# Kernel optimization log

Hardware: AMD Instinct MI355X
Metric: run time of the kernel (lower is better)

## Reference

```python
import jax, jax.numpy as jnp
import numpy as np

E = 1024
H = 8
D = E // H
B = 16384
LN_EPS = 1e-5


def setup_inputs() -> dict:
    key = jax.random.key(0)
    ks = jax.random.split(key, 12)
    s = 1.0 / np.sqrt(E)
    return {
        "image_features": jax.random.normal(ks[0], (B, E), jnp.float32),
        "signal_features": jax.random.normal(ks[1], (B, E), jnp.float32),
        "Wq": jax.random.normal(ks[2], (E, E), jnp.float32) * s,
        "Wk": jax.random.normal(ks[3], (E, E), jnp.float32) * s,
        "Wv": jax.random.normal(ks[4], (E, E), jnp.float32) * s,
        "bq": jnp.zeros((E,), jnp.float32),
        "bk": jnp.zeros((E,), jnp.float32),
        "bv": jnp.zeros((E,), jnp.float32),
        "Wo": jax.random.normal(ks[5], (E, E), jnp.float32) * s,
        "bo": jnp.zeros((E,), jnp.float32),
        "ln_gamma": jnp.ones((E,), jnp.float32),
        "ln_beta": jnp.zeros((E,), jnp.float32),
    }


def _forward(image_features, signal_features, Wq, Wk, Wv, bq, bk, bv, Wo, bo, ln_gamma, ln_beta):
    # query: [B,1,E] from image; key/value: [B,2,E] stacked modalities
    kv = jnp.stack([image_features, signal_features], axis=1)  # [B,2,E]
    # projections (torch Linear convention: x @ W^T + b)
    q = (image_features @ Wq.T + bq).reshape(B, H, 1, D)       # [B,H,1,D]
    k = (kv @ Wk.T + bk).reshape(B, 2, H, D).transpose(0, 2, 1, 3)  # [B,H,2,D]
    v = (kv @ Wv.T + bv).reshape(B, 2, H, D).transpose(0, 2, 1, 3)  # [B,H,2,D]
    scale = 1.0 / jnp.sqrt(jnp.float32(D))
    scores = jnp.einsum("bhqd,bhkd->bhqk", q, k) * scale       # [B,H,1,2]
    attn = jax.nn.softmax(scores, axis=-1)
    ctx = jnp.einsum("bhqk,bhkd->bhqd", attn, v)               # [B,H,1,D]
    ctx = ctx.reshape(B, E)
    attn_out = ctx @ Wo.T + bo
    # residual + LayerNorm (dropout is identity in eval)
    fused = attn_out + image_features
    mu = jnp.mean(fused, axis=-1, keepdims=True)
    var = jnp.var(fused, axis=-1, keepdims=True)
    normed = (fused - mu) * jax.lax.rsqrt(var + LN_EPS)
    return normed * ln_gamma + ln_beta


def reference(image_features, signal_features, Wq, Wk, Wv, bq, bk, bv, Wo, bo, ln_gamma, ln_beta):
    return _forward(image_features, signal_features, Wq, Wk, Wv, bq, bk, bv, Wo, bo, ln_gamma, ln_beta)
```

## Files before the change

### kernel.cpp

```cpp
#include <hip/hip_runtime.h>

#define B_ 16384
#define E_ 1024
#define H_ 8
#define D_ 128

typedef _Float16 f16;
typedef _Float16 f16x8 __attribute__((ext_vector_type(8)));
typedef float f32x4 __attribute__((ext_vector_type(4)));

__device__ __forceinline__ void gload16(const f16* g, f16* l) {
    __builtin_amdgcn_global_load_lds(
        (const __attribute__((address_space(1))) void*)g,
        (__attribute__((address_space(3))) void*)l, 16, 0, 0);
}


__global__ __launch_bounds__(256) void cvt2_kernel(const float4* __restrict__ s0,
                                                   const float4* __restrict__ s1,
                                                   ushort4* __restrict__ d0,
                                                   ushort4* __restrict__ d1, int n4) {
    const float4* s = blockIdx.y ? s1 : s0;
    ushort4* d = blockIdx.y ? d1 : d0;
    int i = blockIdx.x * 256 + threadIdx.x;
    if (i >= n4) return;
    float4 v = s[i];
    union { ushort4 u; f16 h[4]; } o;
    o.h[0] = (f16)v.x; o.h[1] = (f16)v.y; o.h[2] = (f16)v.z; o.h[3] = (f16)v.w;
    d[i] = o.u;
}

__global__ __launch_bounds__(256) void cvt4_kernel(
    const float4* __restrict__ s0, const float4* __restrict__ s1,
    const float4* __restrict__ s2, const float4* __restrict__ s3,
    ushort4* __restrict__ d0, ushort4* __restrict__ d1,
    ushort4* __restrict__ d2, ushort4* __restrict__ d3, int n4) {
    const float4* s; ushort4* d;
    switch (blockIdx.y) {
        case 0: s = s0; d = d0; break;
        case 1: s = s1; d = d1; break;
        case 2: s = s2; d = d2; break;
        default: s = s3; d = d3; break;
    }
    int i = blockIdx.x * 256 + threadIdx.x;
    if (i >= n4) return;
    float4 v = s[i];
    union { ushort4 u; f16 h[4]; } o;
    o.h[0] = (f16)v.x; o.h[1] = (f16)v.y; o.h[2] = (f16)v.z; o.h[3] = (f16)v.w;
    d[i] = o.u;
}

__global__ __launch_bounds__(256, 2) void qkv_attn_kernel(
    const f16* __restrict__ Xi, const f16* __restrict__ Xs,
    const f16* __restrict__ Wq, const f16* __restrict__ Wk, const f16* __restrict__ Wv,
    const float* __restrict__ bq, const float* __restrict__ bk, const float* __restrict__ bv,
    f16* __restrict__ ctx)
{
    (void)bk;
    __shared__ f16 sAi[2][64][32];
    __shared__ f16 sAs[2][64][32];
    __shared__ f16 sWq[2][128][32];
    __shared__ f16 sWk[2][128][32];
    __shared__ f16 sWv[2][128][32];
    __shared__ float sdot[64][2];
    __shared__ float sa0[64];

    const int tid  = threadIdx.x;
    const int lane = tid & 63;
    const int wave = tid >> 6;
    const int wr = wave >> 1, wc = wave & 1;
    const int l16 = lane & 15, lq = lane >> 4;

    const int bid  = blockIdx.x;
    const int head = bid & 7;
    const int row0 = (bid >> 3) * 64;
    const int col0 = head * D_;

    const int lr = lane >> 2;
    const int lc = ((lane & 3) ^ ((lane >> 3) & 3)) * 8;
    const int rc = (lq ^ ((l16 >> 1) & 3)) * 8;

    const f16* gAi = Xi + (size_t)(row0 + wave * 16 + lr) * E_ + lc;
    const f16* gAs = Xs + (size_t)(row0 + wave * 16 + lr) * E_ + lc;
    const size_t woff = (size_t)(col0 + wave * 32 + lr) * E_ + lc;
    const f16* gWq = Wq + woff;
    const f16* gWk = Wk + woff;
    const f16* gWv = Wv + woff;
    const size_t wskip = (size_t)16 * E_;

    f32x4 zero4 = {0.f, 0.f, 0.f, 0.f};
    f32x4 accQ[2][4], accKd[2][4], accVd[2][4], accVs[2][4];
    #pragma unroll
    for (int i = 0; i < 2; i++)
        #pragma unroll
        for (int j = 0; j < 4; j++) {
            accQ[i][j] = zero4; accKd[i][j] = zero4;
            accVd[i][j] = zero4; accVs[i][j] = zero4;
        }

    for (int kk = 0; kk < E_; kk += 64) {
        #pragma unroll
        for (int h = 0; h < 2; h++) {
            const int ko = kk + h * 32;
            gload16(gAi + ko,         &sAi[h][wave * 16][0]);
            gload16(gAs + ko,         &sAs[h][wave * 16][0]);
            gload16(gWq + ko,         &sWq[h][wave * 32][0]);
            gload16(gWq + wskip + ko, &sWq[h][wave * 32 + 16][0]);
            gload16(gWk + ko,         &sWk[h][wave * 32][0]);
            gload16(gWk + wskip + ko, &sWk[h][wave * 32 + 16][0]);
            gload16(gWv + ko,         &sWv[h][wave * 32][0]);
            gload16(gWv + wskip + ko, &sWv[h][wave * 32 + 16][0]);
        }
        __syncthreads();

        #pragma unroll
        for (int h = 0; h < 2; h++) {
            f16x8 aI[2], aS[2], aD[2], bF[4];
            #pragma unroll
            for (int fr = 0; fr < 2; fr++) {
                aI[fr] = *(const f16x8*)&sAi[h][wr * 32 + fr * 16 + l16][rc];
                aS[fr] = *(const f16x8*)&sAs[h][wr * 32 + fr * 16 + l16][rc];
                aD[fr] = aI[fr] - aS[fr];
            }
            #pragma unroll
            for (int fc = 0; fc < 4; fc++)
                bF[fc] = *(const f16x8*)&sWq[h][wc * 64 + fc * 16 + l16][rc];
            #pragma unroll
            for (int fr = 0; fr < 2; fr++)
                #pragma unroll
                for (int fc = 0; fc < 4; fc++)
                    accQ[fr][fc] = __builtin_amdgcn_mfma_f32_16x16x32_f16(aI[fr], bF[fc], accQ[fr][fc], 0, 0, 0);
            #pragma unroll
            for (int fc = 0; fc < 4; fc++)
                bF[fc] = *(const f16x8*)&sWk[h][wc * 64 + fc * 16 + l16][rc];
            #pragma unroll
            for (int fr = 0; fr < 2; fr++)
                #pragma unroll
                for (int fc = 0; fc < 4; fc++)
                    accKd[fr][fc] = __builtin_amdgcn_mfma_f32_16x16x32_f16(aD[fr], bF[fc], accKd[fr][fc], 0, 0, 0);
            #pragma unroll
            for (int fc = 0; fc < 4; fc++)
                bF[fc] = *(const f16x8*)&sWv[h][wc * 64 + fc * 16 + l16][rc];
            #pragma unroll
            for (int fr = 0; fr < 2; fr++)
                #pragma unroll
                for (int fc = 0; fc < 4; fc++) {
                    accVs[fr][fc] = __builtin_amdgcn_mfma_f32_16x16x32_f16(aS[fr], bF[fc], accVs[fr][fc], 0, 0, 0);
                    accVd[fr][fc] = __builtin_amdgcn_mfma_f32_16x16x32_f16(aD[fr], bF[fc], accVd[fr][fc], 0, 0, 0);
                }
        }
        __syncthreads();
    }

    #pragma unroll
    for (int fc = 0; fc < 4; fc++) {
        int col = col0 + wc * 64 + fc * 16 + l16;
        float bqv = bq[col];
        #pragma unroll
        for (int fr = 0; fr < 2; fr++)
            #pragma unroll
            for (int e = 0; e < 4; e++)
                accQ[fr][fc][e] += bqv;
    }

    #pragma unroll
    for (int fr = 0; fr < 2; fr++)
        #pragma unroll
        for (int e = 0; e < 4; e++) {
            float d = 0.f;
            #pragma unroll
            for (int fc = 0; fc < 4; fc++)
                d += accQ[fr][fc][e] * accKd[fr][fc][e];
            #pragma unroll
            for (int m = 1; m < 16; m <<= 1)
                d += __shfl_xor(d, m, 64);
            if (l16 == 0) {
                int row = wr * 32 + fr * 16 + lq * 4 + e;
                sdot[row][wc] = d;
            }
        }
    __syncthreads();
    if (tid < 64) {
        const float scale = 0.088388347648318447f;
        float delta = (sdot[tid][0] + sdot[tid][1]) * scale;
        sa0[tid] = 1.0f / (1.0f + expf(-delta));
    }
    __syncthreads();

    #pragma unroll
    for (int fc = 0; fc < 4; fc++) {
        int col = col0 + wc * 64 + fc * 16 + l16;
        float bvv = bv[col];
        #pragma unroll
        for (int fr = 0; fr < 2; fr++)
            #pragma unroll
            for (int e = 0; e < 4; e++) {
                int row = wr * 32 + fr * 16 + lq * 4 + e;
                float a0 = sa0[row];
                float v  = fmaf(a0, accVd[fr][fc][e], accVs[fr][fc][e]) + bvv;
                ctx[(size_t)(row0 + row) * E_ + col] = (f16)v;
            }
    }
}

__global__ __launch_bounds__(256, 4) void out_proj_kernel(
    const f16* __restrict__ A, const f16* __restrict__ Wo, const float* __restrict__ bo,
    f16* __restrict__ a16)
{
    __shared__ f16 sA[2][128][32];
    __shared__ f16 sB[2][128][32];
    const int tid  = threadIdx.x;
    const int lane = tid & 63;
    const int wave = tid >> 6;
    const int wr = wave >> 1, wc = wave & 1;
    const int l16 = lane & 15, lq = lane >> 4;

    const int bid  = blockIdx.x;
    const int col0 = (bid & 7) * 128;
    const int row0 = (bid >> 3) * 128;

    const int lr = lane >> 2;
    const int lc = ((lane & 3) ^ ((lane >> 3) & 3)) * 8;
    const int rc = (lq ^ ((l16 >> 1) & 3)) * 8;

    const f16* gA0 = A  + (size_t)(row0 + wave * 32 + lr) * E_ + lc;
    const f16* gB0 = Wo + (size_t)(col0 + wave * 32 + lr) * E_ + lc;
    const size_t wskip = (size_t)16 * E_;

    f32x4 zero4 = {0.f, 0.f, 0.f, 0.f};
    f32x4 acc[4][4];
    #pragma unroll
    for (int i = 0; i < 4; i++)
        #pragma unroll
        for (int j = 0; j < 4; j++) acc[i][j] = zero4;

    for (int kk = 0; kk < E_; kk += 64) {
        #pragma unroll
        for (int h = 0; h < 2; h++) {
            const int ko = kk + h * 32;
            gload16(gA0 + ko,         &sA[h][wave * 32][0]);
            gload16(gA0 + wskip + ko, &sA[h][wave * 32 + 16][0]);
            gload16(gB0 + ko,         &sB[h][wave * 32][0]);
            gload16(gB0 + wskip + ko, &sB[h][wave * 32 + 16][0]);
        }
        __syncthreads();

        #pragma unroll
        for (int h = 0; h < 2; h++) {
            f16x8 aF[4], bF[4];
            #pragma unroll
            for (int f = 0; f < 4; f++) {
                aF[f] = *(const f16x8*)&sA[h][wr * 64 + f * 16 + l16][rc];
                bF[f] = *(const f16x8*)&sB[h][wc * 64 + f * 16 + l16][rc];
            }
            #pragma unroll
            for (int fr = 0; fr < 4; fr++)
                #pragma unroll
                for (int fc = 0; fc < 4; fc++)
                    acc[fr][fc] = __builtin_amdgcn_mfma_f32_16x16x32_f16(aF[fr], bF[fc], acc[fr][fc], 0, 0, 0);
        }
        __syncthreads();
    }

    #pragma unroll
    for (int fc = 0; fc < 4; fc++) {
        int col = col0 + wc * 64 + fc * 16 + l16;
        float bov = bo[col];
        #pragma unroll
        for (int fr = 0; fr < 4; fr++)
            #pragma unroll
            for (int e = 0; e < 4; e++) {
                int row = row0 + wr * 64 + fr * 16 + lq * 4 + e;
                a16[(size_t)row * E_ + col] = (f16)(acc[fr][fc][e] + bov);
            }
    }
}

__global__ __launch_bounds__(256) void ln_kernel(
    const f16* __restrict__ a16, const f16* __restrict__ resid16,
    const float* __restrict__ gamma, const float* __restrict__ beta,
    float* __restrict__ out)
{
    const int row = blockIdx.x;
    const int tid = threadIdx.x;
    union { ushort4 u; f16 h[4]; } ua, ur;
    ua.u = ((const ushort4*)(a16     + (size_t)row * E_))[tid];
    ur.u = ((const ushort4*)(resid16 + (size_t)row * E_))[tid];
    float4 v;
    v.x = (float)ua.h[0] + (float)ur.h[0];
    v.y = (float)ua.h[1] + (float)ur.h[1];
    v.z = (float)ua.h[2] + (float)ur.h[2];
    v.w = (float)ua.h[3] + (float)ur.h[3];
    float s  = v.x + v.y + v.z + v.w;
    float s2 = v.x * v.x + v.y * v.y + v.z * v.z + v.w * v.w;
    #pragma unroll
    for (int m = 1; m < 64; m <<= 1) {
        s  += __shfl_xor(s, m, 64);
        s2 += __shfl_xor(s2, m, 64);
    }
    __shared__ float red[8];
    int wv = tid >> 6, ln = tid & 63;
    if (ln == 0) { red[wv] = s; red[4 + wv] = s2; }
    __syncthreads();
    s  = red[0] + red[1] + red[2] + red[3];
    s2 = red[4] + red[5] + red[6] + red[7];
    float mu  = s * (1.0f / E_);
    float var = s2 * (1.0f / E_) - mu * mu;
    float r   = rsqrtf(var + 1e-5f);
    float4 g  = ((const float4*)gamma)[tid];
    float4 bb = ((const float4*)beta)[tid];
    float4 o;
    o.x = (v.x - mu) * r * g.x + bb.x;
    o.y = (v.y - mu) * r * g.y + bb.y;
    o.z = (v.z - mu) * r * g.z + bb.z;
    o.w = (v.w - mu) * r * g.w + bb.w;
    ((float4*)(out + (size_t)row * E_))[tid] = o;
}

extern "C" void kernel_launch(void* const* d_in, const int* in_sizes, int n_in,
                              void* d_out, int out_size, void* d_ws, size_t ws_size,
                              hipStream_t stream)
{
    (void)in_sizes; (void)n_in; (void)out_size; (void)ws_size;
    const float* image  = (const float*)d_in[0];
    const float* signal = (const float*)d_in[1];
    const float* Wq = (const float*)d_in[2];
    const float* Wk = (const float*)d_in[3];
    const float* Wv = (const float*)d_in[4];
    const float* bq = (const float*)d_in[5];
    const float* bk = (const float*)d_in[6];
    const float* bv = (const float*)d_in[7];
    const float* Wo = (const float*)d_in[8];
    const float* bo = (const float*)d_in[9];
    const float* gamma = (const float*)d_in[10];
    const float* beta  = (const float*)d_in[11];
    float* out = (float*)d_out;

    char* ws = (char*)d_ws;
    f16* Xi16 = (f16*)(ws);
    f16* Xs16 = (f16*)(ws + 32ull * 1024 * 1024);
    f16* Wq16 = (f16*)(ws + 64ull * 1024 * 1024);
    f16* Wk16 = (f16*)(ws + 66ull * 1024 * 1024);
    f16* Wv16 = (f16*)(ws + 68ull * 1024 * 1024);
    f16* Wo16 = (f16*)(ws + 70ull * 1024 * 1024);
    f16* ctx  = (f16*)(ws + 72ull * 1024 * 1024);
    f16* a16  = Xs16;

    const int nBE4 = B_ * E_ / 4;
    const int nEE4 = E_ * E_ / 4;
    dim3 gX(nBE4 / 256, 2);
    cvt2_kernel<<<gX, 256, 0, stream>>>((const float4*)image, (const float4*)signal,
                                        (ushort4*)Xi16, (ushort4*)Xs16, nBE4);
    dim3 gW(nEE4 / 256, 4);
    cvt4_kernel<<<gW, 256, 0, stream>>>((const float4*)Wq, (const float4*)Wk,
                                        (const float4*)Wv, (const float4*)Wo,
                                        (ushort4*)Wq16, (ushort4*)Wk16,
                                        (ushort4*)Wv16, (ushort4*)Wo16, nEE4);

    qkv_attn_kernel<<<B_ / 64 * H_, 256, 0, stream>>>(Xi16, Xs16, Wq16, Wk16, Wv16,
                                                      bq, bk, bv, ctx);

    out_proj_kernel<<<B_ / 128 * 8, 256, 0, stream>>>(ctx, Wo16, bo, a16);

    ln_kernel<<<B_, 256, 0, stream>>>(a16, Xi16, gamma, beta, out);
}
```

Before: 430.4 us.

## Fuse fp32-to-fp16 activation conversion into QKV GEMM tile loads

Removes the separate conversion kernel for image and signal features. The QKV kernel now reads fp32 activations directly, converts them in registers and writes swizzled fp16 tiles to LDS. LayerNorm reads the fp32 residual. The grid changes to 2D, putting heads on blockIdx.y, which changes block scheduling order and how the activation tiles are shared across the 8 head blocks in L2. This removes the 64MB read plus 32MB write conversion pass. The cost is that each of the 8 head blocks rereads fp32 activations at twice the bytes and loses the async global_load_lds path for those tiles.

Measured after the change: 446.6 us. +3.8%, slower.

```diff
diff --git a/kernel.cpp b/kernel.cpp
--- a/kernel.cpp
+++ b/kernel.cpp
@@ -15,20 +15,6 @@
         (__attribute__((address_space(3))) void*)l, 16, 0, 0);
 }
 
-
-__global__ __launch_bounds__(256) void cvt2_kernel(const float4* __restrict__ s0,
-                                                   const float4* __restrict__ s1,
-                                                   ushort4* __restrict__ d0,
-                                                   ushort4* __restrict__ d1, int n4) {
-    const float4* s = blockIdx.y ? s1 : s0;
-    ushort4* d = blockIdx.y ? d1 : d0;
-    int i = blockIdx.x * 256 + threadIdx.x;
-    if (i >= n4) return;
-    float4 v = s[i];
-    union { ushort4 u; f16 h[4]; } o;
-    o.h[0] = (f16)v.x; o.h[1] = (f16)v.y; o.h[2] = (f16)v.z; o.h[3] = (f16)v.w;
-    d[i] = o.u;
-}
 
 __global__ __launch_bounds__(256) void cvt4_kernel(
     const float4* __restrict__ s0, const float4* __restrict__ s1,
@@ -51,7 +37,7 @@
 }
 
 __global__ __launch_bounds__(256, 2) void qkv_attn_kernel(
-    const f16* __restrict__ Xi, const f16* __restrict__ Xs,
+    const float* __restrict__ Xi, const float* __restrict__ Xs,
     const f16* __restrict__ Wq, const f16* __restrict__ Wk, const f16* __restrict__ Wv,
     const float* __restrict__ bq, const float* __restrict__ bk, const float* __restrict__ bv,
     f16* __restrict__ ctx)
@@ -71,17 +57,18 @@
     const int wr = wave >> 1, wc = wave & 1;
     const int l16 = lane & 15, lq = lane >> 4;
 
-    const int bid  = blockIdx.x;
-    const int head = bid & 7;
-    const int row0 = (bid >> 3) * 64;
-    const int col0 = head * D_;
+    const int row0 = blockIdx.x * 64;
+    const int col0 = blockIdx.y * D_;
 
     const int lr = lane >> 2;
     const int lc = ((lane & 3) ^ ((lane >> 3) & 3)) * 8;
     const int rc = (lq ^ ((l16 >> 1) & 3)) * 8;
 
-    const f16* gAi = Xi + (size_t)(row0 + wave * 16 + lr) * E_ + lc;
-    const f16* gAs = Xs + (size_t)(row0 + wave * 16 + lr) * E_ + lc;
+    const int xchunk = ((lane & 3) ^ ((lr >> 1) & 3)) * 8;
+    const float* gAif = Xi + (size_t)(row0 + wave * 16 + lr) * E_ + xchunk;
+    const float* gAsf = Xs + (size_t)(row0 + wave * 16 + lr) * E_ + xchunk;
+    const int ldst = (lane & 3) * 8;
+
     const size_t woff = (size_t)(col0 + wave * 32 + lr) * E_ + lc;
     const f16* gWq = Wq + woff;
     const f16* gWk = Wk + woff;
@@ -102,14 +89,27 @@
         #pragma unroll
         for (int h = 0; h < 2; h++) {
             const int ko = kk + h * 32;
-            gload16(gAi + ko,         &sAi[h][wave * 16][0]);
-            gload16(gAs + ko,         &sAs[h][wave * 16][0]);
             gload16(gWq + ko,         &sWq[h][wave * 32][0]);
             gload16(gWq + wskip + ko, &sWq[h][wave * 32 + 16][0]);
             gload16(gWk + ko,         &sWk[h][wave * 32][0]);
             gload16(gWk + wskip + ko, &sWk[h][wave * 32 + 16][0]);
             gload16(gWv + ko,         &sWv[h][wave * 32][0]);
             gload16(gWv + wskip + ko, &sWv[h][wave * 32 + 16][0]);
+        }
+        #pragma unroll
+        for (int h = 0; h < 2; h++) {
+            const int ko = kk + h * 32;
+            float4 i0 = *(const float4*)&gAif[ko];
+            float4 i1 = *(const float4*)&gAif[ko + 4];
+            float4 s0 = *(const float4*)&gAsf[ko];
+            float4 s1 = *(const float4*)&gAsf[ko + 4];
+            union { uint4 u; f16 hh[8]; } ui, us;
+            ui.hh[0] = (f16)i0.x; ui.hh[1] = (f16)i0.y; ui.hh[2] = (f16)i0.z; ui.hh[3] = (f16)i0.w;
+            ui.hh[4] = (f16)i1.x; ui.hh[5] = (f16)i1.y; ui.hh[6] = (f16)i1.z; ui.hh[7] = (f16)i1.w;
+            us.hh[0] = (f16)s0.x; us.hh[1] = (f16)s0.y; us.hh[2] = (f16)s0.z; us.hh[3] = (f16)s0.w;
+            us.hh[4] = (f16)s1.x; us.hh[5] = (f16)s1.y; us.hh[6] = (f16)s1.z; us.hh[7] = (f16)s1.w;
+            *(uint4*)&sAi[h][wave * 16 + lr][ldst] = ui.u;
+            *(uint4*)&sAs[h][wave * 16 + lr][ldst] = us.u;
         }
         __syncthreads();
 
@@ -277,20 +277,20 @@
 }
 
 __global__ __launch_bounds__(256) void ln_kernel(
-    const f16* __restrict__ a16, const f16* __restrict__ resid16,
+    const f16* __restrict__ a16, const float* __restrict__ resid,
     const float* __restrict__ gamma, const float* __restrict__ beta,
     float* __restrict__ out)
 {
     const int row = blockIdx.x;
     const int tid = threadIdx.x;
-    union { ushort4 u; f16 h[4]; } ua, ur;
-    ua.u = ((const ushort4*)(a16     + (size_t)row * E_))[tid];
-    ur.u = ((const ushort4*)(resid16 + (size_t)row * E_))[tid];
+    union { ushort4 u; f16 h[4]; } ua;
+    ua.u = ((const ushort4*)(a16 + (size_t)row * E_))[tid];
+    float4 rv = ((const float4*)(resid + (size_t)row * E_))[tid];
     float4 v;
-    v.x = (float)ua.h[0] + (float)ur.h[0];
-    v.y = (float)ua.h[1] + (float)ur.h[1];
-    v.z = (float)ua.h[2] + (float)ur.h[2];
-    v.w = (float)ua.h[3] + (float)ur.h[3];
+    v.x = (float)ua.h[0] + rv.x;
+    v.y = (float)ua.h[1] + rv.y;
+    v.z = (float)ua.h[2] + rv.z;
+    v.w = (float)ua.h[3] + rv.w;
     float s  = v.x + v.y + v.z + v.w;
     float s2 = v.x * v.x + v.y * v.y + v.z * v.z + v.w * v.w;
     #pragma unroll
@@ -337,30 +337,25 @@
     float* out = (float*)d_out;
 
     char* ws = (char*)d_ws;
-    f16* Xi16 = (f16*)(ws);
-    f16* Xs16 = (f16*)(ws + 32ull * 1024 * 1024);
-    f16* Wq16 = (f16*)(ws + 64ull * 1024 * 1024);
-    f16* Wk16 = (f16*)(ws + 66ull * 1024 * 1024);
-    f16* Wv16 = (f16*)(ws + 68ull * 1024 * 1024);
-    f16* Wo16 = (f16*)(ws + 70ull * 1024 * 1024);
-    f16* ctx  = (f16*)(ws + 72ull * 1024 * 1024);
-    f16* a16  = Xs16;
-
-    const int nBE4 = B_ * E_ / 4;
+    f16* Wq16 = (f16*)(ws);
+    f16* Wk16 = (f16*)(ws + 2ull  * 1024 * 1024);
+    f16* Wv16 = (f16*)(ws + 4ull  * 1024 * 1024);
+    f16* Wo16 = (f16*)(ws + 6ull  * 1024 * 1024);
+    f16* ctx  = (f16*)(ws + 8ull  * 1024 * 1024);
+    f16* a16  = (f16*)(ws + 40ull * 1024 * 1024);
+
     const int nEE4 = E_ * E_ / 4;
-    dim3 gX(nBE4 / 256, 2);
-    cvt2_kernel<<<gX, 256, 0, stream>>>((const float4*)image, (const float4*)signal,
-                                        (ushort4*)Xi16, (ushort4*)Xs16, nBE4);
     dim3 gW(nEE4 / 256, 4);
     cvt4_kernel<<<gW, 256, 0, stream>>>((const float4*)Wq, (const float4*)Wk,
                                         (const float4*)Wv, (const float4*)Wo,
                                         (ushort4*)Wq16, (ushort4*)Wk16,
                                         (ushort4*)Wv16, (ushort4*)Wo16, nEE4);
 
-    qkv_attn_kernel<<<B_ / 64 * H_, 256, 0, stream>>>(Xi16, Xs16, Wq16, Wk16, Wv16,
-                                                      bq, bk, bv, ctx);
+    dim3 g2(B_ / 64, H_);
+    qkv_attn_kernel<<<g2, 256, 0, stream>>>(image, signal, Wq16, Wk16, Wv16,
+                                            bq, bk, bv, ctx);
 
     out_proj_kernel<<<B_ / 128 * 8, 256, 0, stream>>>(ctx, Wo16, bo, a16);
 
-    ln_kernel<<<B_, 256, 0, stream>>>(a16, Xi16, gamma, beta, out);
-}
+    ln_kernel<<<B_, 256, 0, stream>>>(a16, image, gamma, beta, out);
+}
```
